# Optimization experiments

Hardware: AMD Instinct MI355X
Metric: run time of the kernel (lower is better)

The kernel has to match this reference:

```python
import jax, jax.numpy as jnp
import numpy as np

N, S, C, K, V = 8, 2048, 4, 512, 64


def setup_inputs() -> dict:
    key = jax.random.key(0)
    kx, ke = jax.random.split(key)
    x = jax.random.normal(kx, (N, S, C, V), dtype=jnp.float32)
    # nn.Parameter(torch.rand(...)) -> uniform [0,1)
    embedding = jax.random.uniform(ke, (C, K, V), dtype=jnp.float32)
    return {"x": x, "embedding": embedding}


def reference(x, embedding):
    n, s, c, v = x.shape
    xf = x.reshape(n * s, c, v)  # (NS, C, V)
    x2 = jnp.sum(xf * xf, axis=-1, keepdims=True)           # (NS, C, 1)
    e2 = jnp.sum(embedding * embedding, axis=-1)            # (C, K)
    xe = jnp.einsum('ncv,ckv->nck', xf, embedding)          # (NS, C, K)
    d2 = x2 - 2.0 * xe + e2[None]                           # (NS, C, K)
    index = jnp.argmin(d2, axis=2)                          # (NS, C)
    # gather: output[n, c] = embedding[c, index[n, c]]
    output = embedding[jnp.arange(c)[None, :], index]       # (NS, C, V)
    output = output.reshape(x.shape)
    out0 = jax.lax.stop_gradient(output - x) + x            # straight-through
    d1 = jax.lax.stop_gradient(x) - output
    out1 = jnp.sum(d1 * d1, axis=3)                         # (N, S, C)
    d2_ = x - jax.lax.stop_gradient(output)
    out2 = jnp.sum(d2_ * d2_, axis=3)                       # (N, S, C)
    return (out0, out1, out2)
```

## Files before the change

### kernel.cpp

```cpp
#include <hip/hip_runtime.h>

#define NROW 16384
#define CCH  4
#define KCB  512
#define VDIM 64

typedef __attribute__((ext_vector_type(8))) short  short8;
typedef __attribute__((ext_vector_type(4))) float  floatx4;

__device__ inline unsigned short bf16h(float v, float* rem) {
    unsigned u = __float_as_uint(v);
    unsigned r = u + 0x7FFFu + ((u >> 16) & 1u);
    unsigned short h = (unsigned short)(r >> 16);
    *rem = v - __uint_as_float((unsigned)h << 16);
    return h;
}
__device__ inline unsigned short bf16r(float v) {
    unsigned u = __float_as_uint(v);
    return (unsigned short)((u + 0x7FFFu + ((u >> 16) & 1u)) >> 16);
}

__global__ __launch_bounds__(512, 4)
void vq_fused(const float* __restrict__ x, const float* __restrict__ emb,
              float* __restrict__ out) {
    extern __shared__ char smem[];
    unsigned short* eh  = (unsigned short*)smem;
    float*          e2s = (float*)(smem + 65536);
    float*          sdm = (float*)(smem + 67584);
    int*            skm = (int*)  (smem + 68096);

    const int tid  = threadIdx.x;
    const int lane = tid & 63;
    const int m    = lane & 15;
    const int quad = lane >> 4;
    const int wave = tid >> 6;
    const int z    = wave >> 2;
    const int wb   = wave & 3;
    const int c    = blockIdx.y;
    const int rbase = blockIdx.x * 64 + wb * 16;

    const float* embc = emb + (size_t)c * (KCB * VDIM);

    {
        const int cb = wave * 64;
        const int koct = m >> 1, half = m & 1;
#pragma unroll
        for (int j = 0; j < 16; ++j) {
            const int g = cb * 16 + j * 64 + lane;
            const float4 t = ((const float4*)embc)[g];
            const int code = cb + j * 4 + quad;
            ushort4 h4;
            h4.x = bf16r(t.x); h4.y = bf16r(t.y);
            h4.z = bf16r(t.z); h4.w = bf16r(t.w);
            const int off = (koct * 512 + (code ^ koct)) * 8 + half * 4;
            *(ushort4*)&eh[off] = h4;
            float s = 0.f;
            s = fmaf(t.x, t.x, s); s = fmaf(t.y, t.y, s);
            s = fmaf(t.z, t.z, s); s = fmaf(t.w, t.w, s);
            s += __shfl_xor(s, 1, 64);
            s += __shfl_xor(s, 2, 64);
            s += __shfl_xor(s, 4, 64);
            s += __shfl_xor(s, 8, 64);
            if (m == 0) e2s[code] = s;
        }
    }

    short8 ah[2], al[2];
    {
        const int row = rbase + m;
        const float4* xr = (const float4*)(x + ((size_t)row * CCH + c) * VDIM);
#pragma unroll
        for (int h = 0; h < 2; ++h) {
            const float4 f0 = xr[h * 8 + quad * 2];
            const float4 f1 = xr[h * 8 + quad * 2 + 1];
            const float fv[8] = {f0.x, f0.y, f0.z, f0.w, f1.x, f1.y, f1.z, f1.w};
            short8 hh, ll;
#pragma unroll
            for (int j = 0; j < 8; ++j) {
                float r, d;
                hh[j] = (short)bf16h(fv[j], &r);
                ll[j] = (short)bf16h(r, &d);
            }
            ah[h] = hh; al[h] = ll;
        }
    }

    __syncthreads();

    float bd[4]; int bkk[4];
#pragma unroll
    for (int j = 0; j < 4; ++j) { bd[j] = 3.4e38f; bkk[j] = 0; }

    const int mq0 = m ^ quad, mq1 = m ^ (quad + 4);
    const int kbase = z * 256;

#pragma unroll 4
    for (int t = 0; t < 16; ++t) {
        const int kb = kbase + t * 16;
        const int code = kb + m;
        const short8 bh0 = *(const short8*)&eh[( quad      * 512 + kb + mq0) * 8];
        const short8 bh1 = *(const short8*)&eh[((quad + 4) * 512 + kb + mq1) * 8];
        const float e2v = e2s[code];

        floatx4 acc0 = {0.f,0.f,0.f,0.f}, acc1 = {0.f,0.f,0.f,0.f};
        acc0 = __builtin_amdgcn_mfma_f32_16x16x32_bf16(ah[0], bh0, acc0, 0, 0, 0);
        acc1 = __builtin_amdgcn_mfma_f32_16x16x32_bf16(al[0], bh0, acc1, 0, 0, 0);
        acc0 = __builtin_amdgcn_mfma_f32_16x16x32_bf16(ah[1], bh1, acc0, 0, 0, 0);
        acc1 = __builtin_amdgcn_mfma_f32_16x16x32_bf16(al[1], bh1, acc1, 0, 0, 0);

#pragma unroll
        for (int j = 0; j < 4; ++j) {
            const float d0 = fmaf(-2.0f, acc0[j] + acc1[j], e2v);
            if (d0 < bd[j]) { bd[j] = d0; bkk[j] = code; }
        }
    }

#pragma unroll
    for (int j = 0; j < 4; ++j) {
        float d = bd[j]; int k = bkk[j];
#pragma unroll
        for (int mask = 1; mask < 16; mask <<= 1) {
            const float od = __shfl_xor(d, mask, 64);
            const int   ok = __shfl_xor(k, mask, 64);
            if (od < d || (od == d && ok < k)) { d = od; k = ok; }
        }
        bd[j] = d; bkk[j] = k;
    }

    if (m == 0) {
#pragma unroll
        for (int j = 0; j < 4; ++j) {
            sdm[(z * 4 + wb) * 16 + quad * 4 + j] = bd[j];
            skm[(z * 4 + wb) * 16 + quad * 4 + j] = bkk[j];
        }
    }
    __syncthreads();

    if (z == 0) {
        const size_t base1 = (size_t)NROW * CCH * VDIM;
        const size_t base2 = base1 + (size_t)NROW * CCH;
#pragma unroll
        for (int j = 0; j < 4; ++j) {
            const int rl = quad * 4 + j;
            const float d0 = sdm[ wb      * 16 + rl];
            const float d1 = sdm[(4 + wb) * 16 + rl];
            const int   k0 = skm[ wb      * 16 + rl];
            const int   k1 = skm[(4 + wb) * 16 + rl];
            const int code = (d1 < d0) ? k1 : k0;
            const int row  = rbase + rl;

            const float4 t4 = ((const float4*)(x + ((size_t)row * CCH + c) * VDIM))[m];
            const float4 e4 = ((const float4*)(embc + (size_t)code * VDIM))[m];
            float4 w;
            w.x = (e4.x - t4.x) + t4.x;
            w.y = (e4.y - t4.y) + t4.y;
            w.z = (e4.z - t4.z) + t4.z;
            w.w = (e4.w - t4.w) + t4.w;
            ((float4*)(out + ((size_t)row * CCH + c) * VDIM))[m] = w;
            float s = 0.f, dx;
            dx = t4.x - e4.x; s = fmaf(dx, dx, s);
            dx = t4.y - e4.y; s = fmaf(dx, dx, s);
            dx = t4.z - e4.z; s = fmaf(dx, dx, s);
            dx = t4.w - e4.w; s = fmaf(dx, dx, s);
            s += __shfl_xor(s, 1, 64);
            s += __shfl_xor(s, 2, 64);
            s += __shfl_xor(s, 4, 64);
            s += __shfl_xor(s, 8, 64);
            if (m == 0) {
                const size_t idx = (size_t)row * CCH + c;
                out[base1 + idx] = s;
                out[base2 + idx] = s;
            }
        }
    }
}

extern "C" void kernel_launch(void* const* d_in, const int* in_sizes, int n_in,
                              void* d_out, int out_size, void* d_ws, size_t ws_size,
                              hipStream_t stream) {
    const float* x   = (const float*)d_in[0];
    const float* emb = (const float*)d_in[1];
    float* out = (float*)d_out;
    const size_t lds_bytes = 65536u + 2048u + 512u + 512u;
    vq_fused<<<dim3(NROW / 64, CCH), dim3(512), lds_bytes, stream>>>(x, emb, out);
}
```

Measured before the change: 96.15 us.

## Process two row tiles per block to amortize codebook staging into LDS

Each block now handles 128 rows in two sequential 64-row passes instead of 64 rows, halving the grid so the bf16 codebook conversion and norm computation into LDS is done once per 128 rows. The codebook staging is also rewritten so each thread converts one full code row with 16-byte LDS stores and computes its norm serially, removing the shuffle reductions. The cost is fewer blocks (512 instead of 1024), an extra barrier per pass, and strided per-thread global reads of the embedding rows during staging.

```diff
diff --git a/kernel.cpp b/kernel.cpp
--- a/kernel.cpp
+++ b/kernel.cpp
@@ -37,139 +37,139 @@
     const int z    = wave >> 2;
     const int wb   = wave & 3;
     const int c    = blockIdx.y;
-    const int rbase = blockIdx.x * 64 + wb * 16;
 
     const float* embc = emb + (size_t)c * (KCB * VDIM);
 
     {
-        const int cb = wave * 64;
-        const int koct = m >> 1, half = m & 1;
+        const int code = tid;
+        const float4* ef = (const float4*)embc + code * 16;
+        float s = 0.f;
 #pragma unroll
-        for (int j = 0; j < 16; ++j) {
-            const int g = cb * 16 + j * 64 + lane;
-            const float4 t = ((const float4*)embc)[g];
-            const int code = cb + j * 4 + quad;
-            ushort4 h4;
-            h4.x = bf16r(t.x); h4.y = bf16r(t.y);
-            h4.z = bf16r(t.z); h4.w = bf16r(t.w);
-            const int off = (koct * 512 + (code ^ koct)) * 8 + half * 4;
-            *(ushort4*)&eh[off] = h4;
-            float s = 0.f;
-            s = fmaf(t.x, t.x, s); s = fmaf(t.y, t.y, s);
-            s = fmaf(t.z, t.z, s); s = fmaf(t.w, t.w, s);
-            s += __shfl_xor(s, 1, 64);
-            s += __shfl_xor(s, 2, 64);
-            s += __shfl_xor(s, 4, 64);
-            s += __shfl_xor(s, 8, 64);
-            if (m == 0) e2s[code] = s;
+        for (int koct = 0; koct < 8; ++koct) {
+            const float4 a = ef[koct * 2], b = ef[koct * 2 + 1];
+            s = fmaf(a.x, a.x, s); s = fmaf(a.y, a.y, s);
+            s = fmaf(a.z, a.z, s); s = fmaf(a.w, a.w, s);
+            s = fmaf(b.x, b.x, s); s = fmaf(b.y, b.y, s);
+            s = fmaf(b.z, b.z, s); s = fmaf(b.w, b.w, s);
+            short8 hv;
+            hv[0] = (short)bf16r(a.x); hv[1] = (short)bf16r(a.y);
+            hv[2] = (short)bf16r(a.z); hv[3] = (short)bf16r(a.w);
+            hv[4] = (short)bf16r(b.x); hv[5] = (short)bf16r(b.y);
+            hv[6] = (short)bf16r(b.z); hv[7] = (short)bf16r(b.w);
+            *(short8*)&eh[(koct * 512 + (code ^ koct)) * 8] = hv;
         }
+        e2s[code] = s;
     }
-
-    short8 ah[2], al[2];
-    {
-        const int row = rbase + m;
-        const float4* xr = (const float4*)(x + ((size_t)row * CCH + c) * VDIM);
-#pragma unroll
-        for (int h = 0; h < 2; ++h) {
-            const float4 f0 = xr[h * 8 + quad * 2];
-            const float4 f1 = xr[h * 8 + quad * 2 + 1];
-            const float fv[8] = {f0.x, f0.y, f0.z, f0.w, f1.x, f1.y, f1.z, f1.w};
-            short8 hh, ll;
-#pragma unroll
-            for (int j = 0; j < 8; ++j) {
-                float r, d;
-                hh[j] = (short)bf16h(fv[j], &r);
-                ll[j] = (short)bf16h(r, &d);
-            }
-            ah[h] = hh; al[h] = ll;
-        }
-    }
-
     __syncthreads();
-
-    float bd[4]; int bkk[4];
-#pragma unroll
-    for (int j = 0; j < 4; ++j) { bd[j] = 3.4e38f; bkk[j] = 0; }
 
     const int mq0 = m ^ quad, mq1 = m ^ (quad + 4);
     const int kbase = z * 256;
+    const size_t base1 = (size_t)NROW * CCH * VDIM;
+    const size_t base2 = base1 + (size_t)NROW * CCH;
+
+    for (int rt = 0; rt < 2; ++rt) {
+        const int rbase = blockIdx.x * 128 + rt * 64 + wb * 16;
+
+        short8 ah[2], al[2];
+        {
+            const int row = rbase + m;
+            const float4* xr = (const float4*)(x + ((size_t)row * CCH + c) * VDIM);
+#pragma unroll
+            for (int h = 0; h < 2; ++h) {
+                const float4 f0 = xr[h * 8 + quad * 2];
+                const float4 f1 = xr[h * 8 + quad * 2 + 1];
+                const float fv[8] = {f0.x, f0.y, f0.z, f0.w, f1.x, f1.y, f1.z, f1.w};
+                short8 hh, ll;
+#pragma unroll
+                for (int j = 0; j < 8; ++j) {
+                    float r, d;
+                    hh[j] = (short)bf16h(fv[j], &r);
+                    ll[j] = (short)bf16h(r, &d);
+                }
+                ah[h] = hh; al[h] = ll;
+            }
+        }
+
+        float bd[4]; int bkk[4];
+#pragma unroll
+        for (int j = 0; j < 4; ++j) { bd[j] = 3.4e38f; bkk[j] = 0; }
 
 #pragma unroll 4
-    for (int t = 0; t < 16; ++t) {
-        const int kb = kbase + t * 16;
-        const int code = kb + m;
-        const short8 bh0 = *(const short8*)&eh[( quad      * 512 + kb + mq0) * 8];
-        const short8 bh1 = *(const short8*)&eh[((quad + 4) * 512 + kb + mq1) * 8];
-        const float e2v = e2s[code];
+        for (int t = 0; t < 16; ++t) {
+            const int kb = kbase + t * 16;
+            const int code = kb + m;
+            const short8 bh0 = *(const short8*)&eh[( quad      * 512 + kb + mq0) * 8];
+            const short8 bh1 = *(const short8*)&eh[((quad + 4) * 512 + kb + mq1) * 8];
+            const float e2v = e2s[code];
 
-        floatx4 acc0 = {0.f,0.f,0.f,0.f}, acc1 = {0.f,0.f,0.f,0.f};
-        acc0 = __builtin_amdgcn_mfma_f32_16x16x32_bf16(ah[0], bh0, acc0, 0, 0, 0);
-        acc1 = __builtin_amdgcn_mfma_f32_16x16x32_bf16(al[0], bh0, acc1, 0, 0, 0);
-        acc0 = __builtin_amdgcn_mfma_f32_16x16x32_bf16(ah[1], bh1, acc0, 0, 0, 0);
-        acc1 = __builtin_amdgcn_mfma_f32_16x16x32_bf16(al[1], bh1, acc1, 0, 0, 0);
+            floatx4 acc0 = {0.f,0.f,0.f,0.f}, acc1 = {0.f,0.f,0.f,0.f};
+            acc0 = __builtin_amdgcn_mfma_f32_16x16x32_bf16(ah[0], bh0, acc0, 0, 0, 0);
+            acc1 = __builtin_amdgcn_mfma_f32_16x16x32_bf16(al[0], bh0, acc1, 0, 0, 0);
+            acc0 = __builtin_amdgcn_mfma_f32_16x16x32_bf16(ah[1], bh1, acc0, 0, 0, 0);
+            acc1 = __builtin_amdgcn_mfma_f32_16x16x32_bf16(al[1], bh1, acc1, 0, 0, 0);
+
+#pragma unroll
+            for (int j = 0; j < 4; ++j) {
+                const float d0 = fmaf(-2.0f, acc0[j] + acc1[j], e2v);
+                if (d0 < bd[j]) { bd[j] = d0; bkk[j] = code; }
+            }
+        }
 
 #pragma unroll
         for (int j = 0; j < 4; ++j) {
-            const float d0 = fmaf(-2.0f, acc0[j] + acc1[j], e2v);
-            if (d0 < bd[j]) { bd[j] = d0; bkk[j] = code; }
+            float d = bd[j]; int k = bkk[j];
+#pragma unroll
+            for (int mask = 1; mask < 16; mask <<= 1) {
+                const float od = __shfl_xor(d, mask, 64);
+                const int   ok = __shfl_xor(k, mask, 64);
+                if (od < d || (od == d && ok < k)) { d = od; k = ok; }
+            }
+            bd[j] = d; bkk[j] = k;
         }
-    }
 
+        __syncthreads();
+        if (m == 0) {
 #pragma unroll
-    for (int j = 0; j < 4; ++j) {
-        float d = bd[j]; int k = bkk[j];
+            for (int j = 0; j < 4; ++j) {
+                sdm[(z * 4 + wb) * 16 + quad * 4 + j] = bd[j];
+                skm[(z * 4 + wb) * 16 + quad * 4 + j] = bkk[j];
+            }
+        }
+        __syncthreads();
+
+        if (z == 0) {
 #pragma unroll
-        for (int mask = 1; mask < 16; mask <<= 1) {
-            const float od = __shfl_xor(d, mask, 64);
-            const int   ok = __shfl_xor(k, mask, 64);
-            if (od < d || (od == d && ok < k)) { d = od; k = ok; }
-        }
-        bd[j] = d; bkk[j] = k;
-    }
+            for (int j = 0; j < 4; ++j) {
+                const int rl = quad * 4 + j;
+                const float d0 = sdm[ wb      * 16 + rl];
+                const float d1 = sdm[(4 + wb) * 16 + rl];
+                const int   k0 = skm[ wb      * 16 + rl];
+                const int   k1 = skm[(4 + wb) * 16 + rl];
+                const int code = (d1 < d0) ? k1 : k0;
+                const int row  = rbase + rl;
 
-    if (m == 0) {
-#pragma unroll
-        for (int j = 0; j < 4; ++j) {
-            sdm[(z * 4 + wb) * 16 + quad * 4 + j] = bd[j];
-            skm[(z * 4 + wb) * 16 + quad * 4 + j] = bkk[j];
-        }
-    }
-    __syncthreads();
-
-    if (z == 0) {
-        const size_t base1 = (size_t)NROW * CCH * VDIM;
-        const size_t base2 = base1 + (size_t)NROW * CCH;
-#pragma unroll
-        for (int j = 0; j < 4; ++j) {
-            const int rl = quad * 4 + j;
-            const float d0 = sdm[ wb      * 16 + rl];
-            const float d1 = sdm[(4 + wb) * 16 + rl];
-            const int   k0 = skm[ wb      * 16 + rl];
-            const int   k1 = skm[(4 + wb) * 16 + rl];
-            const int code = (d1 < d0) ? k1 : k0;
-            const int row  = rbase + rl;
-
-            const float4 t4 = ((const float4*)(x + ((size_t)row * CCH + c) * VDIM))[m];
-            const float4 e4 = ((const float4*)(embc + (size_t)code * VDIM))[m];
-            float4 w;
-            w.x = (e4.x - t4.x) + t4.x;
-            w.y = (e4.y - t4.y) + t4.y;
-            w.z = (e4.z - t4.z) + t4.z;
-            w.w = (e4.w - t4.w) + t4.w;
-            ((float4*)(out + ((size_t)row * CCH + c) * VDIM))[m] = w;
-            float s = 0.f, dx;
-            dx = t4.x - e4.x; s = fmaf(dx, dx, s);
-            dx = t4.y - e4.y; s = fmaf(dx, dx, s);
-            dx = t4.z - e4.z; s = fmaf(dx, dx, s);
-            dx = t4.w - e4.w; s = fmaf(dx, dx, s);
-            s += __shfl_xor(s, 1, 64);
-            s += __shfl_xor(s, 2, 64);
-            s += __shfl_xor(s, 4, 64);
-            s += __shfl_xor(s, 8, 64);
-            if (m == 0) {
-                const size_t idx = (size_t)row * CCH + c;
-                out[base1 + idx] = s;
-                out[base2 + idx] = s;
+                const float4 t4 = ((const float4*)(x + ((size_t)row * CCH + c) * VDIM))[m];
+                const float4 e4 = ((const float4*)(embc + (size_t)code * VDIM))[m];
+                float4 w;
+                w.x = (e4.x - t4.x) + t4.x;
+                w.y = (e4.y - t4.y) + t4.y;
+                w.z = (e4.z - t4.z) + t4.z;
+                w.w = (e4.w - t4.w) + t4.w;
+                ((float4*)(out + ((size_t)row * CCH + c) * VDIM))[m] = w;
+                float s = 0.f, dx;
+                dx = t4.x - e4.x; s = fmaf(dx, dx, s);
+                dx = t4.y - e4.y; s = fmaf(dx, dx, s);
+                dx = t4.z - e4.z; s = fmaf(dx, dx, s);
+                dx = t4.w - e4.w; s = fmaf(dx, dx, s);
+                s += __shfl_xor(s, 1, 64);
+                s += __shfl_xor(s, 2, 64);
+                s += __shfl_xor(s, 4, 64);
+                s += __shfl_xor(s, 8, 64);
+                if (m == 0) {
+                    const size_t idx = (size_t)row * CCH + c;
+                    out[base1 + idx] = s;
+                    out[base2 + idx] = s;
+                }
             }
         }
     }
@@ -182,5 +182,5 @@
     const float* emb = (const float*)d_in[1];
     float* out = (float*)d_out;
     const size_t lds_bytes = 65536u + 2048u + 512u + 512u;
-    vq_fused<<<dim3(NROW / 64, CCH), dim3(512), lds_bytes, stream>>>(x, emb, out);
+    vq_fused<<<dim3(NROW / 128, CCH), dim3(512), lds_bytes, stream>>>(x, emb, out);
 }
```

Result: faster. 90.66 us (-5.7%).
